# Performance work log

Hardware: AMD Instinct MI355X
Metric: run time of the kernel (lower is better)

Reference implementation:

```python
import jax, jax.numpy as jnp
import numpy as np

S, B, I, H, O = 4096, 64, 14, 256, 1


def _lstm_layer(xs, W_ih, W_hh, b_ih, b_hh, h, c):
    # Precompute input contribution for all timesteps in one big GEMM.
    # xs: [S, B, D_in] -> pre: [S, B, 4H]  (PyTorch gate order: i, f, g, o)
    pre = jnp.einsum('sbd,gd->sbg', xs, W_ih) + b_ih + b_hh

    def step(carry, px):
        h, c = carry
        gates = px + h @ W_hh.T  # [B, 4H]
        i, f, g, o = jnp.split(gates, 4, axis=-1)
        i = jax.nn.sigmoid(i)
        f = jax.nn.sigmoid(f)
        g = jnp.tanh(g)
        o = jax.nn.sigmoid(o)
        c = f * c + i * g
        h = o * jnp.tanh(c)
        return (h, c), h

    (_, _), hs = jax.lax.scan(step, (h, c), pre)
    return hs  # [S, B, H]


def setup_inputs() -> dict:
    key = jax.random.key(0)
    ks = jax.random.split(key, 14)
    s = 1.0 / np.sqrt(H)  # PyTorch LSTM init scale
    u = lambda k, shape: jax.random.uniform(k, shape, jnp.float32, -s, s)
    return {
        'x': jax.random.normal(ks[0], (S, B, I), jnp.float32),
        'h0': jax.random.normal(ks[1], (2, B, H), jnp.float32),
        'c0': jax.random.normal(ks[2], (2, B, H), jnp.float32),
        'W_ih0': u(ks[3], (4 * H, I)),
        'W_hh0': u(ks[4], (4 * H, H)),
        'b_ih0': u(ks[5], (4 * H,)),
        'b_hh0': u(ks[6], (4 * H,)),
        'W_ih1': u(ks[7], (4 * H, H)),
        'W_hh1': u(ks[8], (4 * H, H)),
        'b_ih1': u(ks[9], (4 * H,)),
        'b_hh1': u(ks[10], (4 * H,)),
        'W_fc': u(ks[11], (O, H)),
        'b_fc': u(ks[12], (O,)),
    }


def reference(x, h0, c0, W_ih0, W_hh0, b_ih0, b_hh0,
              W_ih1, W_hh1, b_ih1, b_hh1, W_fc, b_fc):
    hs0 = _lstm_layer(x, W_ih0, W_hh0, b_ih0, b_hh0, h0[0], c0[0])
    # dropout=0.4 between layers applies only in train mode; eval reference -> identity
    hs1 = _lstm_layer(hs0, W_ih1, W_hh1, b_ih1, b_hh1, h0[1], c0[1])
    out = jax.nn.relu(hs1)
    return out @ W_fc.T + b_fc  # [S, B, O]
```

## Files before the change

kernel.cpp:

```cpp
#include <hip/hip_runtime.h>


#define S_LEN 4096
#define BATCH 64
#define IN_DIM 14
#define HID 256
#define GATES 1024
#define K0 288
#define LDA0 296
#define K1 512
#define LDA1 520
#define GST 261

typedef _Float16 half8 __attribute__((ext_vector_type(8)));
typedef float f32x4 __attribute__((ext_vector_type(4)));
typedef unsigned long long u64;
typedef unsigned int u32;

__device__ __forceinline__ float sigf(float z) { return 1.0f / (1.0f + __expf(-z)); }
__device__ __forceinline__ float tanhf2(float z) { return 2.0f / (1.0f + __expf(-2.0f * z)) - 1.0f; }

__device__ __forceinline__ u32 packh2(float a, float b) {
    union { _Float16 h[2]; u32 u; } q;
    q.h[0] = (_Float16)a; q.h[1] = (_Float16)b;
    return q.u;
}

__device__ __forceinline__ u32 ld32_c(const u32* p) {
    u32 r;
    asm volatile("global_load_dword %0, %1, off sc0 sc1\n\ts_waitcnt vmcnt(0)"
                 : "=&v"(r) : "v"(p) : "memory");
    return r;
}
__device__ __forceinline__ void st32_c(u32* p, u32 v) {
    asm volatile("global_store_dword %0, %1, off sc0 sc1" :: "v"(p), "v"(v) : "memory");
}
__device__ __forceinline__ void st64_c(u64* p, u64 v) {
    asm volatile("global_store_dwordx2 %0, %1, off sc0 sc1" :: "v"(p), "v"(v) : "memory");
}
__device__ __forceinline__ void ld64x3_c(const u64* p0, const u64* p1, const u64* p2,
                                         u64& r0, u64& r1, u64& r2) {
    asm volatile(
        "global_load_dwordx2 %0, %3, off sc0 sc1\n\t"
        "global_load_dwordx2 %1, %4, off sc0 sc1\n\t"
        "global_load_dwordx2 %2, %5, off sc0 sc1\n\t"
        "s_waitcnt vmcnt(0)"
        : "=&v"(r0), "=&v"(r1), "=&v"(r2)
        : "v"(p0), "v"(p1), "v"(p2)
        : "memory");
}
__device__ __forceinline__ void ld64x7_c(
    const u64* a0, const u64* a1, const u64* a2, const u64* a3,
    const u64* p0, const u64* p1, const u64* p2,
    u64& q0, u64& q1, u64& q2, u64& q3, u64& v0, u64& v1, u64& v2) {
    asm volatile(
        "global_load_dwordx2 %0, %7, off sc0 sc1\n\t"
        "global_load_dwordx2 %1, %8, off sc0 sc1\n\t"
        "global_load_dwordx2 %2, %9, off sc0 sc1\n\t"
        "global_load_dwordx2 %3, %10, off sc0 sc1\n\t"
        "global_load_dwordx2 %4, %11, off sc0 sc1\n\t"
        "global_load_dwordx2 %5, %12, off sc0 sc1\n\t"
        "global_load_dwordx2 %6, %13, off sc0 sc1\n\t"
        "s_waitcnt vmcnt(0)"
        : "=&v"(q0), "=&v"(q1), "=&v"(q2), "=&v"(q3), "=&v"(v0), "=&v"(v1), "=&v"(v2)
        : "v"(a0), "v"(a1), "v"(a2), "v"(a3), "v"(p0), "v"(p1), "v"(p2)
        : "memory");
}

__global__ void prep_weights(const float* __restrict__ Wih0, const float* __restrict__ Whh0,
                             const float* __restrict__ bih0, const float* __restrict__ bhh0,
                             const float* __restrict__ Wih1, const float* __restrict__ Whh1,
                             const float* __restrict__ bih1, const float* __restrict__ bhh1,
                             _Float16* __restrict__ wcat0, _Float16* __restrict__ wcat1,
                             float* __restrict__ b0, float* __restrict__ b1) {
    int idx0 = blockIdx.x * blockDim.x + threadIdx.x;
    int stride = gridDim.x * blockDim.x;
    for (int i = idx0; i < GATES * K0; i += stride) {
        int n = i / K0, k = i % K0;
        float v = 0.f;
        if (k < HID) v = Whh0[n * HID + k];
        else if (k < HID + IN_DIM) v = Wih0[n * IN_DIM + (k - HID)];
        wcat0[i] = (_Float16)v;
    }
    for (int i = idx0; i < GATES * K1; i += stride) {
        int n = i / K1, k = i % K1;
        float v = (k < HID) ? Whh1[n * HID + k] : Wih1[n * HID + (k - HID)];
        wcat1[i] = (_Float16)v;
    }
    for (int i = idx0; i < GATES; i += stride) {
        b0[i] = bih0[i] + bhh0[i];
        b1[i] = bih1[i] + bhh1[i];
    }
}

__global__ __launch_bounds__(512) void lstm_scan(
    const float* __restrict__ x, const float* __restrict__ h0g, const float* __restrict__ c0g,
    const _Float16* __restrict__ wcat0, const _Float16* __restrict__ wcat1,
    const float* __restrict__ b0, const float* __restrict__ b1,
    const float* __restrict__ wfc, const float* __restrict__ bfc,
    u64* __restrict__ h0ring, u64* __restrict__ h1ring,
    u32* __restrict__ prog, float* __restrict__ out, int R0) {
    const int bi = blockIdx.x;
    const int x7 = bi & 7;
    const int g = x7 >> 1;
    const int sub = ((x7 & 1) << 2) | (bi >> 3);
    const int L = sub >> 2;
    const int j = sub & 3;

    const int tid = threadIdx.x;
    const int w = tid >> 6;
    const int lane = tid & 63;
    const int quad = lane >> 4;
    const int col = lane & 15;
    const int c0b = g * 16;
    const int pm = tid & 15;
    const int iu = tid >> 4;
    const int pu = iu * 2;
    const int gm = tid >> 5;
    const int gu = tid & 31;

    __shared__ __align__(16) _Float16 Ash[16 * LDA1];
    __shared__ float Gsh[16 * GST];
    __shared__ float WfS[HID];
    __shared__ u32 OwnH[512];

    u64* h0w = h0ring + (size_t)g * R0 * 2048;
    u64* h1w = h1ring + (size_t)g * 4 * 2048;
    const int R0m = R0 - 1;

    int peer[3];
    { int c = 0; for (int p = 0; p < 4; ++p) if (p != j) peer[c++] = p; }

    int gbudget = 1 << 22;

    if (L == 0) {
        half8 wr[2][K0 / 32];
        float bs[2];
#pragma unroll
        for (int tt = 0; tt < 2; ++tt) {
            int t = w + 8 * tt;
            int n = (t >> 2) * 256 + j * 64 + (t & 3) * 16 + col;
            bs[tt] = b0[n];
            const _Float16* wp = wcat0 + (size_t)n * K0 + quad * 8;
#pragma unroll
            for (int kk = 0; kk < K0 / 32; ++kk) wr[tt][kk] = *(const half8*)(wp + kk * 32);
        }
        float cs0 = c0g[(size_t)(c0b + pm) * HID + j * 64 + pu];
        float cs1 = c0g[(size_t)(c0b + pm) * HID + j * 64 + pu + 1];
        {
            int m = tid >> 5, cw = tid & 31;
            const float* hp = h0g + (size_t)(c0b + m) * HID + cw * 8;
            half8 hv;
#pragma unroll
            for (int q2 = 0; q2 < 8; ++q2) hv[q2] = (_Float16)hp[q2];
            *(half8*)&Ash[m * LDA0 + cw * 8] = hv;
            if (cw >= IN_DIM) Ash[m * LDA0 + HID + cw] = (_Float16)0.f;
        }
        const int xm = tid / IN_DIM, xd = tid - xm * IN_DIM;
        if (tid < 16 * IN_DIM)
            Ash[xm * LDA0 + HID + xd] = (_Float16)x[(size_t)(c0b + xm) * IN_DIM + xd];
        __syncthreads();

        for (int s = 0; s < S_LEN; ++s) {
            float xpre = 0.f;
            if (tid < 16 * IN_DIM && s + 1 < S_LEN)
                xpre = x[((size_t)(s + 1) * BATCH + c0b + xm) * IN_DIM + xd];
            if (w == 0 && lane < 4 && (s & 7) == 0 && s + 10 > R0) {
                const u32* np = prog + g * 4 + lane;
                int tgt = s + 10 - R0;
                while ((int)ld32_c(np) < tgt && --gbudget > 0) __builtin_amdgcn_s_sleep(4);
            }
            if (s > 0) {
                const u64* base = h0w + (size_t)((s - 1) & R0m) * 2048;
                const u64* p0 = base + peer[0] * 512 + tid;
                const u64* p1 = base + peer[1] * 512 + tid;
                const u64* p2 = base + peer[2] * 512 + tid;
                u64 v0, v1, v2;
                ld64x3_c(p0, p1, p2, v0, v1, v2);
                const u32 tg = (u32)s;
                while ((((u32)(v0 >> 32) != tg) | ((u32)(v1 >> 32) != tg) |
                        ((u32)(v2 >> 32) != tg)) && --gbudget > 0)
                    ld64x3_c(p0, p1, p2, v0, v1, v2);
                *(u32*)&Ash[gm * LDA0 + peer[0] * 64 + 2 * gu] = (u32)v0;
                *(u32*)&Ash[gm * LDA0 + peer[1] * 64 + 2 * gu] = (u32)v1;
                *(u32*)&Ash[gm * LDA0 + peer[2] * 64 + 2 * gu] = (u32)v2;
            }
            __syncthreads();
            f32x4 acc0 = {bs[0], bs[0], bs[0], bs[0]};
            f32x4 acc1 = {bs[1], bs[1], bs[1], bs[1]};
#pragma unroll
            for (int kk = 0; kk < K0 / 32; ++kk) {
                half8 av = *(const half8*)&Ash[col * LDA0 + kk * 32 + quad * 8];
                acc0 = __builtin_amdgcn_mfma_f32_16x16x32_f16(av, wr[0][kk], acc0, 0, 0, 0);
                acc1 = __builtin_amdgcn_mfma_f32_16x16x32_f16(av, wr[1][kk], acc1, 0, 0, 0);
            }
#pragma unroll
            for (int r = 0; r < 4; ++r) {
                Gsh[(quad * 4 + r) * GST + w * 16 + col] = acc0[r];
                Gsh[(quad * 4 + r) * GST + (w + 8) * 16 + col] = acc1[r];
            }
            __syncthreads();
            {
                float iv = sigf(Gsh[pm * GST + pu]);
                float fv = sigf(Gsh[pm * GST + 64 + pu]);
                float gv = tanhf2(Gsh[pm * GST + 128 + pu]);
                float ov = sigf(Gsh[pm * GST + 192 + pu]);
                cs0 = fv * cs0 + iv * gv;
                float ha = ov * tanhf2(cs0);
                iv = sigf(Gsh[pm * GST + pu + 1]);
                fv = sigf(Gsh[pm * GST + 64 + pu + 1]);
                gv = tanhf2(Gsh[pm * GST + 128 + pu + 1]);
                ov = sigf(Gsh[pm * GST + 192 + pu + 1]);
                cs1 = fv * cs1 + iv * gv;
                float hb = ov * tanhf2(cs1);
                u32 hw = packh2(ha, hb);
                *(u32*)&Ash[pm * LDA0 + j * 64 + pu] = hw;
                st64_c(h0w + (size_t)(s & R0m) * 2048 + j * 512 + (pm * 32 + iu),
                       (u64)hw | ((u64)(u32)(s + 1) << 32));
            }
            if (tid < 16 * IN_DIM && s + 1 < S_LEN)
                Ash[xm * LDA0 + HID + xd] = (_Float16)xpre;
        }
    } else {
        half8 wr[2][K1 / 32];
        float bs[2];
#pragma unroll
        for (int tt = 0; tt < 2; ++tt) {
            int t = w + 8 * tt;
            int n = (t >> 2) * 256 + j * 64 + (t & 3) * 16 + col;
            bs[tt] = b1[n];
            const _Float16* wp = wcat1 + (size_t)n * K1 + quad * 8;
#pragma unroll
            for (int kk = 0; kk < K1 / 32; ++kk) wr[tt][kk] = *(const half8*)(wp + kk * 32);
        }
        for (int i = tid; i < HID; i += 512) WfS[i] = wfc[i];
        const float bfcv = bfc[0];
        float cs0 = c0g[(size_t)(BATCH + c0b + pm) * HID + j * 64 + pu];
        float cs1 = c0g[(size_t)(BATCH + c0b + pm) * HID + j * 64 + pu + 1];
        {
            int m = tid >> 5, cw = tid & 31;
            const float* hp = h0g + (size_t)(BATCH + c0b + m) * HID + cw * 8;
            half8 hv;
#pragma unroll
            for (int q2 = 0; q2 < 8; ++q2) hv[q2] = (_Float16)hp[q2];
            *(half8*)&Ash[m * LDA1 + cw * 8] = hv;
        }
        u32* progself = prog + g * 4 + j;
        __syncthreads();

        for (int s = 0; s <= S_LEN; ++s) {
            if (w == 7 && s >= 2) {
                int m = 4 * j + quad;
                float fa = 0.f;
#pragma unroll
                for (int k16 = 0; k16 < 16; ++k16) {
                    float hv = (float)Ash[m * LDA1 + col + 16 * k16];
                    fa += fmaxf(hv, 0.f) * WfS[col + 16 * k16];
                }
#pragma unroll
                for (int off = 1; off < 16; off <<= 1) fa += __shfl_xor(fa, off, 16);
                if (col == 0) out[(size_t)(s - 2) * BATCH + c0b + m] = fa + bfcv;
            }
            const u64* hb = h0w + (size_t)((s < S_LEN ? s : 0) & R0m) * 2048;
            const u64* a0 = hb + tid;
            const u64* a1 = hb + 512 + tid;
            const u64* a2 = hb + 1024 + tid;
            const u64* a3 = hb + 1536 + tid;
            const u64* pb = h1w + (size_t)(((s > 0 ? s : 1) - 1) & 3) * 2048;
            const u64* p0 = pb + peer[0] * 512 + tid;
            const u64* p1 = pb + peer[1] * 512 + tid;
            const u64* p2 = pb + peer[2] * 512 + tid;
            u64 q0, q1, q2, q3, v0, v1, v2;
            ld64x7_c(a0, a1, a2, a3, p0, p1, p2, q0, q1, q2, q3, v0, v1, v2);
            {
                const u32 tgq = (u32)(s + 1), tgv = (u32)s;
                for (;;) {
                    bool bad = false;
                    if (s < S_LEN)
                        bad |= ((u32)(q0 >> 32) != tgq) | ((u32)(q1 >> 32) != tgq) |
                               ((u32)(q2 >> 32) != tgq) | ((u32)(q3 >> 32) != tgq);
                    if (s > 0)
                        bad |= ((u32)(v0 >> 32) != tgv) | ((u32)(v1 >> 32) != tgv) |
                               ((u32)(v2 >> 32) != tgv);
                    if (!bad || --gbudget <= 0) break;
                    ld64x7_c(a0, a1, a2, a3, p0, p1, p2, q0, q1, q2, q3, v0, v1, v2);
                }
            }
            __syncthreads();
            if (s > 0) {
                *(u32*)&Ash[gm * LDA1 + peer[0] * 64 + 2 * gu] = (u32)v0;
                *(u32*)&Ash[gm * LDA1 + peer[1] * 64 + 2 * gu] = (u32)v1;
                *(u32*)&Ash[gm * LDA1 + peer[2] * 64 + 2 * gu] = (u32)v2;
                *(u32*)&Ash[gm * LDA1 + j * 64 + 2 * gu] = OwnH[tid];
            }
            if (s < S_LEN) {
                *(u32*)&Ash[gm * LDA1 + HID + 0 * 64 + 2 * gu] = (u32)q0;
                *(u32*)&Ash[gm * LDA1 + HID + 1 * 64 + 2 * gu] = (u32)q1;
                *(u32*)&Ash[gm * LDA1 + HID + 2 * 64 + 2 * gu] = (u32)q2;
                *(u32*)&Ash[gm * LDA1 + HID + 3 * 64 + 2 * gu] = (u32)q3;
            }
            __syncthreads();
            if (s == S_LEN) {
                if (w == 7) {
                    int m = 4 * j + quad;
                    float fa = 0.f;
#pragma unroll
                    for (int k16 = 0; k16 < 16; ++k16) {
                        float hv = (float)Ash[m * LDA1 + col + 16 * k16];
                        fa += fmaxf(hv, 0.f) * WfS[col + 16 * k16];
                    }
#pragma unroll
                    for (int off = 1; off < 16; off <<= 1) fa += __shfl_xor(fa, off, 16);
                    if (col == 0) out[(size_t)(S_LEN - 1) * BATCH + c0b + m] = fa + bfcv;
                }
                break;
            }
            f32x4 acc0 = {bs[0], bs[0], bs[0], bs[0]};
            f32x4 acc1 = {bs[1], bs[1], bs[1], bs[1]};
#pragma unroll
            for (int kk = 0; kk < K1 / 32; ++kk) {
                half8 av = *(const half8*)&Ash[col * LDA1 + kk * 32 + quad * 8];
                acc0 = __builtin_amdgcn_mfma_f32_16x16x32_f16(av, wr[0][kk], acc0, 0, 0, 0);
                acc1 = __builtin_amdgcn_mfma_f32_16x16x32_f16(av, wr[1][kk], acc1, 0, 0, 0);
            }
#pragma unroll
            for (int r = 0; r < 4; ++r) {
                Gsh[(quad * 4 + r) * GST + w * 16 + col] = acc0[r];
                Gsh[(quad * 4 + r) * GST + (w + 8) * 16 + col] = acc1[r];
            }
            __syncthreads();
            {
                float iv = sigf(Gsh[pm * GST + pu]);
                float fv = sigf(Gsh[pm * GST + 64 + pu]);
                float gv = tanhf2(Gsh[pm * GST + 128 + pu]);
                float ov = sigf(Gsh[pm * GST + 192 + pu]);
                cs0 = fv * cs0 + iv * gv;
                float ha = ov * tanhf2(cs0);
                iv = sigf(Gsh[pm * GST + pu + 1]);
                fv = sigf(Gsh[pm * GST + 64 + pu + 1]);
                gv = tanhf2(Gsh[pm * GST + 128 + pu + 1]);
                ov = sigf(Gsh[pm * GST + 192 + pu + 1]);
                cs1 = fv * cs1 + iv * gv;
                float hb = ov * tanhf2(cs1);
                u32 hw = packh2(ha, hb);
                OwnH[pm * 32 + iu] = hw;
                st64_c(h1w + (size_t)(s & 3) * 2048 + j * 512 + (pm * 32 + iu),
                       (u64)hw | ((u64)(u32)(s + 1) << 32));
            }
            if ((s & 7) == 7 && tid == 0) st32_c(progself, (u32)(s + 1));
            __syncthreads();
        }
    }
}

extern "C" void kernel_launch(void* const* d_in, const int* in_sizes, int n_in,
                              void* d_out, int out_size, void* d_ws, size_t ws_size,
                              hipStream_t stream) {
    const float* x    = (const float*)d_in[0];
    const float* h0   = (const float*)d_in[1];
    const float* c0   = (const float*)d_in[2];
    const float* Wih0 = (const float*)d_in[3];
    const float* Whh0 = (const float*)d_in[4];
    const float* bih0 = (const float*)d_in[5];
    const float* bhh0 = (const float*)d_in[6];
    const float* Wih1 = (const float*)d_in[7];
    const float* Whh1 = (const float*)d_in[8];
    const float* bih1 = (const float*)d_in[9];
    const float* bhh1 = (const float*)d_in[10];
    const float* Wfc  = (const float*)d_in[11];
    const float* bfc  = (const float*)d_in[12];
    float* out = (float*)d_out;

    char* ws = (char*)d_ws;
    constexpr size_t OFF_WCAT0 = 0;
    constexpr size_t SZ_WCAT0 = (size_t)GATES * K0 * 2;
    constexpr size_t OFF_WCAT1 = OFF_WCAT0 + SZ_WCAT0;
    constexpr size_t SZ_WCAT1 = (size_t)GATES * K1 * 2;
    constexpr size_t OFF_B0 = OFF_WCAT1 + SZ_WCAT1;
    constexpr size_t OFF_B1 = OFF_B0 + 4096;
    constexpr size_t OFF_PROG = OFF_B1 + 4096;
    constexpr size_t OFF_H1R = OFF_PROG + 4096;
    constexpr size_t SZ_H1R = (size_t)4 * 4 * 2048 * 8;
    constexpr size_t OFF_H0R = OFF_H1R + SZ_H1R;

    _Float16* wcat0 = (_Float16*)(ws + OFF_WCAT0);
    _Float16* wcat1 = (_Float16*)(ws + OFF_WCAT1);
    float* b0 = (float*)(ws + OFF_B0);
    float* b1 = (float*)(ws + OFF_B1);
    u32* prog = (u32*)(ws + OFF_PROG);
    u64* h1ring = (u64*)(ws + OFF_H1R);

    int R0 = 128;
    while (OFF_H0R + (size_t)4 * R0 * 2048 * 8 > ws_size && R0 > 16) R0 >>= 1;
    u64* h0ring = (u64*)(ws + OFF_H0R);

    hipMemsetAsync(ws + OFF_PROG, 0,
                   (OFF_H0R - OFF_PROG) + (size_t)4 * R0 * 2048 * 8, stream);
    prep_weights<<<256, 256, 0, stream>>>(Wih0, Whh0, bih0, bhh0, Wih1, Whh1, bih1, bhh1,
                                          wcat0, wcat1, b0, b1);
    lstm_scan<<<32, 512, 0, stream>>>(x, h0, c0, wcat0, wcat1, b0, b1, Wfc, bfc,
                                      h0ring, h1ring, prog, out, R0);
}
```

Before: 10.26 ms.

## Split layer-1 recurrence loads and overlap peer exchange with input-half MFMAs

```diff
diff --git a/kernel.cpp b/kernel.cpp
--- a/kernel.cpp
+++ b/kernel.cpp
@@ -26,6 +26,12 @@
     return q.u;
 }
 
+#define VMWAIT() do { asm volatile("s_waitcnt vmcnt(0)" ::: "memory"); \
+                      __builtin_amdgcn_sched_barrier(0); } while (0)
+#define BARX()   do { asm volatile("s_waitcnt lgkmcnt(0)" ::: "memory"); \
+                      __builtin_amdgcn_s_barrier(); \
+                      asm volatile("" ::: "memory"); } while (0)
+
 __device__ __forceinline__ u32 ld32_c(const u32* p) {
     u32 r;
     asm volatile("global_load_dword %0, %1, off sc0 sc1\n\ts_waitcnt vmcnt(0)"
@@ -49,21 +55,37 @@
         : "v"(p0), "v"(p1), "v"(p2)
         : "memory");
 }
-__device__ __forceinline__ void ld64x7_c(
-    const u64* a0, const u64* a1, const u64* a2, const u64* a3,
-    const u64* p0, const u64* p1, const u64* p2,
-    u64& q0, u64& q1, u64& q2, u64& q3, u64& v0, u64& v1, u64& v2) {
+__device__ __forceinline__ void ld64x4_c(const u64* p0, const u64* p1, const u64* p2,
+                                         const u64* p3, u64& r0, u64& r1, u64& r2, u64& r3) {
     asm volatile(
-        "global_load_dwordx2 %0, %7, off sc0 sc1\n\t"
-        "global_load_dwordx2 %1, %8, off sc0 sc1\n\t"
-        "global_load_dwordx2 %2, %9, off sc0 sc1\n\t"
-        "global_load_dwordx2 %3, %10, off sc0 sc1\n\t"
-        "global_load_dwordx2 %4, %11, off sc0 sc1\n\t"
-        "global_load_dwordx2 %5, %12, off sc0 sc1\n\t"
-        "global_load_dwordx2 %6, %13, off sc0 sc1\n\t"
+        "global_load_dwordx2 %0, %4, off sc0 sc1\n\t"
+        "global_load_dwordx2 %1, %5, off sc0 sc1\n\t"
+        "global_load_dwordx2 %2, %6, off sc0 sc1\n\t"
+        "global_load_dwordx2 %3, %7, off sc0 sc1\n\t"
         "s_waitcnt vmcnt(0)"
-        : "=&v"(q0), "=&v"(q1), "=&v"(q2), "=&v"(q3), "=&v"(v0), "=&v"(v1), "=&v"(v2)
-        : "v"(a0), "v"(a1), "v"(a2), "v"(a3), "v"(p0), "v"(p1), "v"(p2)
+        : "=&v"(r0), "=&v"(r1), "=&v"(r2), "=&v"(r3)
+        : "v"(p0), "v"(p1), "v"(p2), "v"(p3)
+        : "memory");
+}
+__device__ __forceinline__ void issue64x3(const u64* p0, const u64* p1, const u64* p2,
+                                          u64& r0, u64& r1, u64& r2) {
+    asm volatile(
+        "global_load_dwordx2 %0, %3, off sc0 sc1\n\t"
+        "global_load_dwordx2 %1, %4, off sc0 sc1\n\t"
+        "global_load_dwordx2 %2, %5, off sc0 sc1"
+        : "=&v"(r0), "=&v"(r1), "=&v"(r2)
+        : "v"(p0), "v"(p1), "v"(p2)
+        : "memory");
+}
+__device__ __forceinline__ void issue64x4(const u64* p0, const u64* p1, const u64* p2,
+                                          const u64* p3, u64& r0, u64& r1, u64& r2, u64& r3) {
+    asm volatile(
+        "global_load_dwordx2 %0, %4, off sc0 sc1\n\t"
+        "global_load_dwordx2 %1, %5, off sc0 sc1\n\t"
+        "global_load_dwordx2 %2, %6, off sc0 sc1\n\t"
+        "global_load_dwordx2 %3, %7, off sc0 sc1"
+        : "=&v"(r0), "=&v"(r1), "=&v"(r2), "=&v"(r3)
+        : "v"(p0), "v"(p1), "v"(p2), "v"(p3)
         : "memory");
 }
 
@@ -248,7 +270,24 @@
         u32* progself = prog + g * 4 + j;
         __syncthreads();
 
-        for (int s = 0; s <= S_LEN; ++s) {
+        const u64 *a0, *a1, *a2, *a3;
+        u64 q0, q1, q2, q3;
+        a0 = h0w + tid;  a1 = h0w + 512 + tid;
+        a2 = h0w + 1024 + tid;  a3 = h0w + 1536 + tid;
+        issue64x4(a0, a1, a2, a3, q0, q1, q2, q3);
+
+        for (int s = 0; s < S_LEN; ++s) {
+            VMWAIT();
+            {
+                const u32 tgq = (u32)(s + 1);
+                while ((((u32)(q0 >> 32) != tgq) | ((u32)(q1 >> 32) != tgq) |
+                        ((u32)(q2 >> 32) != tgq) | ((u32)(q3 >> 32) != tgq)) && --gbudget > 0)
+                    ld64x4_c(a0, a1, a2, a3, q0, q1, q2, q3);
+                *(u32*)&Ash[gm * LDA1 + HID + 0 * 64 + 2 * gu] = (u32)q0;
+                *(u32*)&Ash[gm * LDA1 + HID + 1 * 64 + 2 * gu] = (u32)q1;
+                *(u32*)&Ash[gm * LDA1 + HID + 2 * 64 + 2 * gu] = (u32)q2;
+                *(u32*)&Ash[gm * LDA1 + HID + 3 * 64 + 2 * gu] = (u32)q3;
+            }
             if (w == 7 && s >= 2) {
                 int m = 4 * j + quad;
                 float fa = 0.f;
@@ -261,64 +300,44 @@
                 for (int off = 1; off < 16; off <<= 1) fa += __shfl_xor(fa, off, 16);
                 if (col == 0) out[(size_t)(s - 2) * BATCH + c0b + m] = fa + bfcv;
             }
-            const u64* hb = h0w + (size_t)((s < S_LEN ? s : 0) & R0m) * 2048;
-            const u64* a0 = hb + tid;
-            const u64* a1 = hb + 512 + tid;
-            const u64* a2 = hb + 1024 + tid;
-            const u64* a3 = hb + 1536 + tid;
-            const u64* pb = h1w + (size_t)(((s > 0 ? s : 1) - 1) & 3) * 2048;
-            const u64* p0 = pb + peer[0] * 512 + tid;
-            const u64* p1 = pb + peer[1] * 512 + tid;
-            const u64* p2 = pb + peer[2] * 512 + tid;
-            u64 q0, q1, q2, q3, v0, v1, v2;
-            ld64x7_c(a0, a1, a2, a3, p0, p1, p2, q0, q1, q2, q3, v0, v1, v2);
-            {
-                const u32 tgq = (u32)(s + 1), tgv = (u32)s;
-                for (;;) {
-                    bool bad = false;
-                    if (s < S_LEN)
-                        bad |= ((u32)(q0 >> 32) != tgq) | ((u32)(q1 >> 32) != tgq) |
-                               ((u32)(q2 >> 32) != tgq) | ((u32)(q3 >> 32) != tgq);
-                    if (s > 0)
-                        bad |= ((u32)(v0 >> 32) != tgv) | ((u32)(v1 >> 32) != tgv) |
-                               ((u32)(v2 >> 32) != tgv);
-                    if (!bad || --gbudget <= 0) break;
-                    ld64x7_c(a0, a1, a2, a3, p0, p1, p2, q0, q1, q2, q3, v0, v1, v2);
-                }
-            }
-            __syncthreads();
+            const u64 *p0 = nullptr, *p1 = nullptr, *p2 = nullptr;
+            u64 v0 = 0, v1 = 0, v2 = 0;
             if (s > 0) {
+                const u64* pb = h1w + (size_t)((s - 1) & 3) * 2048;
+                p0 = pb + peer[0] * 512 + tid;
+                p1 = pb + peer[1] * 512 + tid;
+                p2 = pb + peer[2] * 512 + tid;
+                issue64x3(p0, p1, p2, v0, v1, v2);
+            }
+            BARX();
+            f32x4 acc0 = {bs[0], bs[0], bs[0], bs[0]};
+            f32x4 acc1 = {bs[1], bs[1], bs[1], bs[1]};
+#pragma unroll
+            for (int kk = 8; kk < 16; ++kk) {
+                half8 av = *(const half8*)&Ash[col * LDA1 + kk * 32 + quad * 8];
+                acc0 = __builtin_amdgcn_mfma_f32_16x16x32_f16(av, wr[0][kk], acc0, 0, 0, 0);
+                acc1 = __builtin_amdgcn_mfma_f32_16x16x32_f16(av, wr[1][kk], acc1, 0, 0, 0);
+            }
+            if (s > 0) {
+                VMWAIT();
+                const u32 tgv = (u32)s;
+                while ((((u32)(v0 >> 32) != tgv) | ((u32)(v1 >> 32) != tgv) |
+                        ((u32)(v2 >> 32) != tgv)) && --gbudget > 0)
+                    ld64x3_c(p0, p1, p2, v0, v1, v2);
                 *(u32*)&Ash[gm * LDA1 + peer[0] * 64 + 2 * gu] = (u32)v0;
                 *(u32*)&Ash[gm * LDA1 + peer[1] * 64 + 2 * gu] = (u32)v1;
                 *(u32*)&Ash[gm * LDA1 + peer[2] * 64 + 2 * gu] = (u32)v2;
                 *(u32*)&Ash[gm * LDA1 + j * 64 + 2 * gu] = OwnH[tid];
             }
-            if (s < S_LEN) {
-                *(u32*)&Ash[gm * LDA1 + HID + 0 * 64 + 2 * gu] = (u32)q0;
-                *(u32*)&Ash[gm * LDA1 + HID + 1 * 64 + 2 * gu] = (u32)q1;
-                *(u32*)&Ash[gm * LDA1 + HID + 2 * 64 + 2 * gu] = (u32)q2;
-                *(u32*)&Ash[gm * LDA1 + HID + 3 * 64 + 2 * gu] = (u32)q3;
-            }
-            __syncthreads();
-            if (s == S_LEN) {
-                if (w == 7) {
-                    int m = 4 * j + quad;
-                    float fa = 0.f;
-#pragma unroll
-                    for (int k16 = 0; k16 < 16; ++k16) {
-                        float hv = (float)Ash[m * LDA1 + col + 16 * k16];
-                        fa += fmaxf(hv, 0.f) * WfS[col + 16 * k16];
-                    }
-#pragma unroll
-                    for (int off = 1; off < 16; off <<= 1) fa += __shfl_xor(fa, off, 16);
-                    if (col == 0) out[(size_t)(S_LEN - 1) * BATCH + c0b + m] = fa + bfcv;
-                }
-                break;
-            }
-            f32x4 acc0 = {bs[0], bs[0], bs[0], bs[0]};
-            f32x4 acc1 = {bs[1], bs[1], bs[1], bs[1]};
-#pragma unroll
-            for (int kk = 0; kk < K1 / 32; ++kk) {
+            BARX();
+            if (s + 1 < S_LEN) {
+                const u64* hb = h0w + (size_t)((s + 1) & R0m) * 2048;
+                a0 = hb + tid;  a1 = hb + 512 + tid;
+                a2 = hb + 1024 + tid;  a3 = hb + 1536 + tid;
+                issue64x4(a0, a1, a2, a3, q0, q1, q2, q3);
+            }
+#pragma unroll
+            for (int kk = 0; kk < 8; ++kk) {
                 half8 av = *(const half8*)&Ash[col * LDA1 + kk * 32 + quad * 8];
                 acc0 = __builtin_amdgcn_mfma_f32_16x16x32_f16(av, wr[0][kk], acc0, 0, 0, 0);
                 acc1 = __builtin_amdgcn_mfma_f32_16x16x32_f16(av, wr[1][kk], acc1, 0, 0, 0);
@@ -328,7 +347,7 @@
                 Gsh[(quad * 4 + r) * GST + w * 16 + col] = acc0[r];
                 Gsh[(quad * 4 + r) * GST + (w + 8) * 16 + col] = acc1[r];
             }
-            __syncthreads();
+            BARX();
             {
                 float iv = sigf(Gsh[pm * GST + pu]);
                 float fv = sigf(Gsh[pm * GST + 64 + pu]);
@@ -348,7 +367,48 @@
                        (u64)hw | ((u64)(u32)(s + 1) << 32));
             }
             if ((s & 7) == 7 && tid == 0) st32_c(progself, (u32)(s + 1));
-            __syncthreads();
+        }
+        if (w == 7) {
+            int m = 4 * j + quad;
+            float fa = 0.f;
+#pragma unroll
+            for (int k16 = 0; k16 < 16; ++k16) {
+                float hv = (float)Ash[m * LDA1 + col + 16 * k16];
+                fa += fmaxf(hv, 0.f) * WfS[col + 16 * k16];
+            }
+#pragma unroll
+            for (int off = 1; off < 16; off <<= 1) fa += __shfl_xor(fa, off, 16);
+            if (col == 0) out[(size_t)(S_LEN - 2) * BATCH + c0b + m] = fa + bfcv;
+        }
+        {
+            const u64* pb = h1w + (size_t)((S_LEN - 1) & 3) * 2048;
+            const u64* p0 = pb + peer[0] * 512 + tid;
+            const u64* p1 = pb + peer[1] * 512 + tid;
+            const u64* p2 = pb + peer[2] * 512 + tid;
+            u64 v0, v1, v2;
+            ld64x3_c(p0, p1, p2, v0, v1, v2);
+            const u32 tgv = (u32)S_LEN;
+            while ((((u32)(v0 >> 32) != tgv) | ((u32)(v1 >> 32) != tgv) |
+                    ((u32)(v2 >> 32) != tgv)) && --gbudget > 0)
+                ld64x3_c(p0, p1, p2, v0, v1, v2);
+            BARX();
+            *(u32*)&Ash[gm * LDA1 + peer[0] * 64 + 2 * gu] = (u32)v0;
+            *(u32*)&Ash[gm * LDA1 + peer[1] * 64 + 2 * gu] = (u32)v1;
+            *(u32*)&Ash[gm * LDA1 + peer[2] * 64 + 2 * gu] = (u32)v2;
+            *(u32*)&Ash[gm * LDA1 + j * 64 + 2 * gu] = OwnH[tid];
+        }
+        BARX();
+        if (w == 7) {
+            int m = 4 * j + quad;
+            float fa = 0.f;
+#pragma unroll
+            for (int k16 = 0; k16 < 16; ++k16) {
+                float hv = (float)Ash[m * LDA1 + col + 16 * k16];
+                fa += fmaxf(hv, 0.f) * WfS[col + 16 * k16];
+            }
+#pragma unroll
+            for (int off = 1; off < 16; off <<= 1) fa += __shfl_xor(fa, off, 16);
+            if (col == 0) out[(size_t)(S_LEN - 1) * BATCH + c0b + m] = fa + bfcv;
         }
     }
 }
```

Result: slower. 11.45 ms (+11.6%).

## Overlap peer hidden-state polling loads with local-slice MFMA and FC work

Applied to the files above, without the earlier changes.

```diff
diff --git a/kernel.cpp b/kernel.cpp
--- a/kernel.cpp
+++ b/kernel.cpp
@@ -25,6 +25,9 @@
     q.h[0] = (_Float16)a; q.h[1] = (_Float16)b;
     return q.u;
 }
+
+#define VMWAIT() do { asm volatile("s_waitcnt vmcnt(0)" ::: "memory"); \
+                      __builtin_amdgcn_sched_barrier(0); } while (0)
 
 __device__ __forceinline__ u32 ld32_c(const u32* p) {
     u32 r;
@@ -62,6 +65,32 @@
         "global_load_dwordx2 %5, %12, off sc0 sc1\n\t"
         "global_load_dwordx2 %6, %13, off sc0 sc1\n\t"
         "s_waitcnt vmcnt(0)"
+        : "=&v"(q0), "=&v"(q1), "=&v"(q2), "=&v"(q3), "=&v"(v0), "=&v"(v1), "=&v"(v2)
+        : "v"(a0), "v"(a1), "v"(a2), "v"(a3), "v"(p0), "v"(p1), "v"(p2)
+        : "memory");
+}
+__device__ __forceinline__ void issue64x3(const u64* p0, const u64* p1, const u64* p2,
+                                          u64& r0, u64& r1, u64& r2) {
+    asm volatile(
+        "global_load_dwordx2 %0, %3, off sc0 sc1\n\t"
+        "global_load_dwordx2 %1, %4, off sc0 sc1\n\t"
+        "global_load_dwordx2 %2, %5, off sc0 sc1"
+        : "=&v"(r0), "=&v"(r1), "=&v"(r2)
+        : "v"(p0), "v"(p1), "v"(p2)
+        : "memory");
+}
+__device__ __forceinline__ void issue64x7(
+    const u64* a0, const u64* a1, const u64* a2, const u64* a3,
+    const u64* p0, const u64* p1, const u64* p2,
+    u64& q0, u64& q1, u64& q2, u64& q3, u64& v0, u64& v1, u64& v2) {
+    asm volatile(
+        "global_load_dwordx2 %0, %7, off sc0 sc1\n\t"
+        "global_load_dwordx2 %1, %8, off sc0 sc1\n\t"
+        "global_load_dwordx2 %2, %9, off sc0 sc1\n\t"
+        "global_load_dwordx2 %3, %10, off sc0 sc1\n\t"
+        "global_load_dwordx2 %4, %11, off sc0 sc1\n\t"
+        "global_load_dwordx2 %5, %12, off sc0 sc1\n\t"
+        "global_load_dwordx2 %6, %13, off sc0 sc1"
         : "=&v"(q0), "=&v"(q1), "=&v"(q2), "=&v"(q3), "=&v"(v0), "=&v"(v1), "=&v"(v2)
         : "v"(a0), "v"(a1), "v"(a2), "v"(a3), "v"(p0), "v"(p1), "v"(p2)
         : "memory");
@@ -162,6 +191,15 @@
         __syncthreads();
 
         for (int s = 0; s < S_LEN; ++s) {
+            const u64 *p0 = nullptr, *p1 = nullptr, *p2 = nullptr;
+            u64 v0 = 0, v1 = 0, v2 = 0;
+            if (s > 0) {
+                const u64* base = h0w + (size_t)((s - 1) & R0m) * 2048;
+                p0 = base + peer[0] * 512 + tid;
+                p1 = base + peer[1] * 512 + tid;
+                p2 = base + peer[2] * 512 + tid;
+                issue64x3(p0, p1, p2, v0, v1, v2);
+            }
             float xpre = 0.f;
             if (tid < 16 * IN_DIM && s + 1 < S_LEN)
                 xpre = x[((size_t)(s + 1) * BATCH + c0b + xm) * IN_DIM + xd];
@@ -170,13 +208,23 @@
                 int tgt = s + 10 - R0;
                 while ((int)ld32_c(np) < tgt && --gbudget > 0) __builtin_amdgcn_s_sleep(4);
             }
+            f32x4 acc0 = {bs[0], bs[0], bs[0], bs[0]};
+            f32x4 acc1 = {bs[1], bs[1], bs[1], bs[1]};
+#pragma unroll
+            for (int kk = 0; kk < 8; ++kk) {
+                if ((kk >> 1) == j) {
+                    half8 av = *(const half8*)&Ash[col * LDA0 + kk * 32 + quad * 8];
+                    acc0 = __builtin_amdgcn_mfma_f32_16x16x32_f16(av, wr[0][kk], acc0, 0, 0, 0);
+                    acc1 = __builtin_amdgcn_mfma_f32_16x16x32_f16(av, wr[1][kk], acc1, 0, 0, 0);
+                }
+            }
+            {
+                half8 av = *(const half8*)&Ash[col * LDA0 + 8 * 32 + quad * 8];
+                acc0 = __builtin_amdgcn_mfma_f32_16x16x32_f16(av, wr[0][8], acc0, 0, 0, 0);
+                acc1 = __builtin_amdgcn_mfma_f32_16x16x32_f16(av, wr[1][8], acc1, 0, 0, 0);
+            }
             if (s > 0) {
-                const u64* base = h0w + (size_t)((s - 1) & R0m) * 2048;
-                const u64* p0 = base + peer[0] * 512 + tid;
-                const u64* p1 = base + peer[1] * 512 + tid;
-                const u64* p2 = base + peer[2] * 512 + tid;
-                u64 v0, v1, v2;
-                ld64x3_c(p0, p1, p2, v0, v1, v2);
+                VMWAIT();
                 const u32 tg = (u32)s;
                 while ((((u32)(v0 >> 32) != tg) | ((u32)(v1 >> 32) != tg) |
                         ((u32)(v2 >> 32) != tg)) && --gbudget > 0)
@@ -186,13 +234,13 @@
                 *(u32*)&Ash[gm * LDA0 + peer[2] * 64 + 2 * gu] = (u32)v2;
             }
             __syncthreads();
-            f32x4 acc0 = {bs[0], bs[0], bs[0], bs[0]};
-            f32x4 acc1 = {bs[1], bs[1], bs[1], bs[1]};
-#pragma unroll
-            for (int kk = 0; kk < K0 / 32; ++kk) {
-                half8 av = *(const half8*)&Ash[col * LDA0 + kk * 32 + quad * 8];
-                acc0 = __builtin_amdgcn_mfma_f32_16x16x32_f16(av, wr[0][kk], acc0, 0, 0, 0);
-                acc1 = __builtin_amdgcn_mfma_f32_16x16x32_f16(av, wr[1][kk], acc1, 0, 0, 0);
+#pragma unroll
+            for (int kk = 0; kk < 8; ++kk) {
+                if ((kk >> 1) != j) {
+                    half8 av = *(const half8*)&Ash[col * LDA0 + kk * 32 + quad * 8];
+                    acc0 = __builtin_amdgcn_mfma_f32_16x16x32_f16(av, wr[0][kk], acc0, 0, 0, 0);
+                    acc1 = __builtin_amdgcn_mfma_f32_16x16x32_f16(av, wr[1][kk], acc1, 0, 0, 0);
+                }
             }
 #pragma unroll
             for (int r = 0; r < 4; ++r) {
@@ -220,6 +268,7 @@
             }
             if (tid < 16 * IN_DIM && s + 1 < S_LEN)
                 Ash[xm * LDA0 + HID + xd] = (_Float16)xpre;
+            __syncthreads();
         }
     } else {
         half8 wr[2][K1 / 32];
@@ -249,18 +298,6 @@
         __syncthreads();
 
         for (int s = 0; s <= S_LEN; ++s) {
-            if (w == 7 && s >= 2) {
-                int m = 4 * j + quad;
-                float fa = 0.f;
-#pragma unroll
-                for (int k16 = 0; k16 < 16; ++k16) {
-                    float hv = (float)Ash[m * LDA1 + col + 16 * k16];
-                    fa += fmaxf(hv, 0.f) * WfS[col + 16 * k16];
-                }
-#pragma unroll
-                for (int off = 1; off < 16; off <<= 1) fa += __shfl_xor(fa, off, 16);
-                if (col == 0) out[(size_t)(s - 2) * BATCH + c0b + m] = fa + bfcv;
-            }
             const u64* hb = h0w + (size_t)((s < S_LEN ? s : 0) & R0m) * 2048;
             const u64* a0 = hb + tid;
             const u64* a1 = hb + 512 + tid;
@@ -271,7 +308,20 @@
             const u64* p1 = pb + peer[1] * 512 + tid;
             const u64* p2 = pb + peer[2] * 512 + tid;
             u64 q0, q1, q2, q3, v0, v1, v2;
-            ld64x7_c(a0, a1, a2, a3, p0, p1, p2, q0, q1, q2, q3, v0, v1, v2);
+            issue64x7(a0, a1, a2, a3, p0, p1, p2, q0, q1, q2, q3, v0, v1, v2);
+            if (w == 7 && s >= 2) {
+                int m = 4 * j + quad;
+                float fa = 0.f;
+#pragma unroll
+                for (int k16 = 0; k16 < 16; ++k16) {
+                    float hv = (float)Ash[m * LDA1 + col + 16 * k16];
+                    fa += fmaxf(hv, 0.f) * WfS[col + 16 * k16];
+                }
+#pragma unroll
+                for (int off = 1; off < 16; off <<= 1) fa += __shfl_xor(fa, off, 16);
+                if (col == 0) out[(size_t)(s - 2) * BATCH + c0b + m] = fa + bfcv;
+            }
+            VMWAIT();
             {
                 const u32 tgq = (u32)(s + 1), tgv = (u32)s;
                 for (;;) {
```

Result: slower. 11.62 ms (+13.3%).
